# Performance work log

Measured on AMD Instinct MI355X. Metric: run time of the kernel, lower is better.

The kernel has to match this reference:

```python
import jax, jax.numpy as jnp
import numpy as np

N_NODES = 100000
N_EDGES = 600000
IN_C, HID_C, OUT_C = 128, 128, 64


def setup_inputs() -> dict:
    key = jax.random.key(0)
    k1, k2, k3, k4 = jax.random.split(key, 4)
    x = jax.random.normal(k1, (N_NODES, IN_C), dtype=jnp.float32)
    edge_index = jax.random.randint(k2, (2, N_EDGES), 0, N_NODES, dtype=jnp.int64)
    # Glorot-ish init for linear weights
    W1 = jax.random.normal(k3, (IN_C, HID_C), dtype=jnp.float32) / np.sqrt(IN_C)
    b1 = jnp.zeros((HID_C,), dtype=jnp.float32)
    W2 = jax.random.normal(k4, (HID_C, OUT_C), dtype=jnp.float32) / np.sqrt(HID_C)
    b2 = jnp.zeros((OUT_C,), dtype=jnp.float32)
    prelu_a = jnp.full((1,), 0.25, dtype=jnp.float32)  # torch nn.PReLU default
    return {"x": x, "edge_index": edge_index, "W1": W1, "b1": b1,
            "W2": W2, "b2": b2, "prelu_a": prelu_a}


def _gcn_conv(x, src, dst, norm, W, b, num_nodes):
    # PyG GCNConv: h = x W; out[i] = sum_{(j->i)} norm_ji * h[j] + b
    h = x @ W                                   # [N, C_out]
    msg = h[src] * norm[:, None]                # [E', C_out] gather + scale
    out = jax.ops.segment_sum(msg, dst, num_segments=num_nodes)
    return out + b


def reference(x, edge_index, W1, b1, W2, b2, prelu_a):
    n = x.shape[0]
    # add self-loops
    loops = jnp.arange(n, dtype=edge_index.dtype)
    src = jnp.concatenate([edge_index[0], loops])
    dst = jnp.concatenate([edge_index[1], loops])
    # symmetric normalization deg^{-1/2}[src] * deg^{-1/2}[dst]
    deg = jax.ops.segment_sum(jnp.ones_like(dst, dtype=x.dtype), dst, num_segments=n)
    dinv = jnp.where(deg > 0, jax.lax.rsqrt(deg), 0.0)
    norm = dinv[src] * dinv[dst]
    # dropout p=0.0 -> identity
    h = _gcn_conv(x, src, dst, norm, W1, b1, n)
    h = jnp.where(h >= 0, h, prelu_a * h)       # PReLU (single shared parameter)
    out = _gcn_conv(h, src, dst, norm, W2, b2, n)
    return out
```

## Files before the change

kernel.cpp:

```cpp
#include <hip/hip_runtime.h>


typedef __attribute__((ext_vector_type(8))) short bf16x8;
typedef __attribute__((ext_vector_type(4))) float f32x4;

#define CAP 32

__device__ inline unsigned short f2bf(float f) {
    unsigned int b = __float_as_uint(f);
    b += 0x7FFFu + ((b >> 16) & 1u);
    return (unsigned short)(b >> 16);
}
__device__ inline float bflo(unsigned int u) { return __uint_as_float(u << 16); }
__device__ inline float bfhi(unsigned int u) { return __uint_as_float(u & 0xFFFF0000u); }

__global__ void k_pre(const float* __restrict__ W1, const float* __restrict__ W2,
                      unsigned short* __restrict__ Wt1, unsigned short* __restrict__ Wt2,
                      int* __restrict__ cnt, int n) {
    int i = blockIdx.x * blockDim.x + threadIdx.x;
    if (i < n) cnt[i] = 0;
    if (i < 128 * 128) {
        int nn = i >> 7, k = i & 127;
        Wt1[i] = f2bf(W1[k * 128 + nn]);
    } else if (i < 128 * 128 + 64 * 128) {
        int j = i - 128 * 128;
        int nn = j >> 7, k = j & 127;
        Wt2[j] = f2bf(W2[k * 64 + nn]);
    }
}

template <int BN, bool CVT, bool FILL>
__global__ __launch_bounds__(512) void k_gemm_mfma(
    const void* __restrict__ Asrc, const unsigned short* __restrict__ Wt,
    unsigned short* __restrict__ H, int n,
    const int* __restrict__ esrc, const int* __restrict__ edst,
    int* __restrict__ cnt, int* __restrict__ bucket, int e) {
    constexpr int PITCH = 136;
    __shared__ unsigned short Bs[BN * PITCH];
    const int tid = threadIdx.x;

    for (int q = tid; q < BN * 16; q += 512) {
        int row = q >> 4, c16 = q & 15;
        *(uint4*)(Bs + row * PITCH + c16 * 8) =
            *(const uint4*)(Wt + row * 128 + c16 * 8);
    }

    const int wave = tid >> 6, lane = tid & 63;
    const int ml = lane & 15;
    const int g = lane >> 4;
    const int stripe = blockIdx.x * 8 + wave;

    int ra = stripe * 16 + ml;
    if (ra >= n) ra = n - 1;

    bf16x8 af[4];
    if (CVT) {
        const float* A = (const float*)Asrc;
#pragma unroll
        for (int ks = 0; ks < 4; ++ks) {
            const float* p = A + (size_t)ra * 128 + ks * 32 + g * 8;
            float4 a0 = *(const float4*)p;
            float4 a1 = *(const float4*)(p + 4);
            uint4 pk;
            pk.x = (unsigned)f2bf(a0.x) | ((unsigned)f2bf(a0.y) << 16);
            pk.y = (unsigned)f2bf(a0.z) | ((unsigned)f2bf(a0.w) << 16);
            pk.z = (unsigned)f2bf(a1.x) | ((unsigned)f2bf(a1.y) << 16);
            pk.w = (unsigned)f2bf(a1.z) | ((unsigned)f2bf(a1.w) << 16);
            af[ks] = *(bf16x8*)&pk;
        }
    } else {
        const unsigned short* A = (const unsigned short*)Asrc;
#pragma unroll
        for (int ks = 0; ks < 4; ++ks)
            af[ks] = *(const bf16x8*)(A + (size_t)ra * 128 + ks * 32 + g * 8);
    }

    if (FILL) {
        for (int i = blockIdx.x * 512 + tid; i < e; i += gridDim.x * 512) {
            int d = edst[i];
            int s = esrc[i];
            int pos = atomicAdd(&cnt[d], 1);
            if (pos < CAP) bucket[(size_t)d * CAP + pos] = s;
        }
    }

    __syncthreads();

    constexpr int NCT = BN / 16;
    f32x4 acc[NCT];
#pragma unroll
    for (int ct = 0; ct < NCT; ++ct) acc[ct] = (f32x4){0.f, 0.f, 0.f, 0.f};

#pragma unroll
    for (int ks = 0; ks < 4; ++ks)
#pragma unroll
        for (int ct = 0; ct < NCT; ++ct) {
            bf16x8 b = *(const bf16x8*)(Bs + (size_t)(ct * 16 + ml) * PITCH + ks * 32 + g * 8);
            acc[ct] = __builtin_amdgcn_mfma_f32_16x16x32_bf16(af[ks], b, acc[ct], 0, 0, 0);
        }

#pragma unroll
    for (int ct = 0; ct < NCT; ++ct)
#pragma unroll
        for (int reg = 0; reg < 4; ++reg) {
            int r = stripe * 16 + g * 4 + reg;
            if (r < n) H[(size_t)r * BN + ct * 16 + ml] = f2bf(acc[ct][reg]);
        }
}

template <int COLS, bool PRELU_BF16_OUT>
__global__ void k_gather(const unsigned short* __restrict__ H,
                         const int* __restrict__ cnt, const int* __restrict__ bucket,
                         const float* __restrict__ b, void* __restrict__ outp,
                         const float* __restrict__ alpha_p, int n) {
    constexpr int NT = COLS / 8;
    constexpr int G = 256 / NT;
    const int tid = threadIdx.x;
    const int node = blockIdx.x * G + tid / NT;
    if (node >= n) return;
    const int c0 = (tid & (NT - 1)) * 8;

    int c = cnt[node];
    const float di = rsqrtf(1.0f + (float)c);
    if (c > CAP) c = CAP;

    float acc[8];
    {
        uint4 v = *(const uint4*)(H + (size_t)node * COLS + c0);
        float sl = di * di;
        acc[0] = bflo(v.x) * sl + b[c0 + 0];
        acc[1] = bfhi(v.x) * sl + b[c0 + 1];
        acc[2] = bflo(v.y) * sl + b[c0 + 2];
        acc[3] = bfhi(v.y) * sl + b[c0 + 3];
        acc[4] = bflo(v.z) * sl + b[c0 + 4];
        acc[5] = bfhi(v.z) * sl + b[c0 + 5];
        acc[6] = bflo(v.w) * sl + b[c0 + 6];
        acc[7] = bfhi(v.w) * sl + b[c0 + 7];
    }

    const int* bp = bucket + (size_t)node * CAP;
    const int nb4 = (c + 3) >> 2;
    for (int q = 0; q < nb4; ++q) {
        int4 idx = *(const int4*)(bp + q * 4);
        int base = q * 4;
        int s0 = idx.x;
        int s1 = (base + 1 < c) ? idx.y : s0;
        int s2 = (base + 2 < c) ? idx.z : s0;
        int s3 = (base + 3 < c) ? idx.w : s0;
        int cn0 = cnt[s0], cn1 = cnt[s1], cn2 = cnt[s2], cn3 = cnt[s3];
        uint4 v0 = *(const uint4*)(H + (size_t)s0 * COLS + c0);
        uint4 v1 = *(const uint4*)(H + (size_t)s1 * COLS + c0);
        uint4 v2 = *(const uint4*)(H + (size_t)s2 * COLS + c0);
        uint4 v3 = *(const uint4*)(H + (size_t)s3 * COLS + c0);
        float n0 = rsqrtf(1.0f + (float)cn0) * di;
        float n1 = (base + 1 < c) ? rsqrtf(1.0f + (float)cn1) * di : 0.0f;
        float n2 = (base + 2 < c) ? rsqrtf(1.0f + (float)cn2) * di : 0.0f;
        float n3 = (base + 3 < c) ? rsqrtf(1.0f + (float)cn3) * di : 0.0f;
        acc[0] += bflo(v0.x) * n0; acc[1] += bfhi(v0.x) * n0;
        acc[2] += bflo(v0.y) * n0; acc[3] += bfhi(v0.y) * n0;
        acc[4] += bflo(v0.z) * n0; acc[5] += bfhi(v0.z) * n0;
        acc[6] += bflo(v0.w) * n0; acc[7] += bfhi(v0.w) * n0;
        acc[0] += bflo(v1.x) * n1; acc[1] += bfhi(v1.x) * n1;
        acc[2] += bflo(v1.y) * n1; acc[3] += bfhi(v1.y) * n1;
        acc[4] += bflo(v1.z) * n1; acc[5] += bfhi(v1.z) * n1;
        acc[6] += bflo(v1.w) * n1; acc[7] += bfhi(v1.w) * n1;
        acc[0] += bflo(v2.x) * n2; acc[1] += bfhi(v2.x) * n2;
        acc[2] += bflo(v2.y) * n2; acc[3] += bfhi(v2.y) * n2;
        acc[4] += bflo(v2.z) * n2; acc[5] += bfhi(v2.z) * n2;
        acc[6] += bflo(v2.w) * n2; acc[7] += bfhi(v2.w) * n2;
        acc[0] += bflo(v3.x) * n3; acc[1] += bfhi(v3.x) * n3;
        acc[2] += bflo(v3.y) * n3; acc[3] += bfhi(v3.y) * n3;
        acc[4] += bflo(v3.z) * n3; acc[5] += bfhi(v3.z) * n3;
        acc[6] += bflo(v3.w) * n3; acc[7] += bfhi(v3.w) * n3;
    }

    if (PRELU_BF16_OUT) {
        float al = alpha_p[0];
        unsigned short o[8];
#pragma unroll
        for (int j = 0; j < 8; ++j) {
            float t = acc[j];
            t = (t >= 0.f) ? t : al * t;
            o[j] = f2bf(t);
        }
        uint4 pk;
        pk.x = (unsigned)o[0] | ((unsigned)o[1] << 16);
        pk.y = (unsigned)o[2] | ((unsigned)o[3] << 16);
        pk.z = (unsigned)o[4] | ((unsigned)o[5] << 16);
        pk.w = (unsigned)o[6] | ((unsigned)o[7] << 16);
        *(uint4*)((unsigned short*)outp + (size_t)node * COLS + c0) = pk;
    } else {
        float* out = (float*)outp;
        *(float4*)(out + (size_t)node * COLS + c0) =
            make_float4(acc[0], acc[1], acc[2], acc[3]);
        *(float4*)(out + (size_t)node * COLS + c0 + 4) =
            make_float4(acc[4], acc[5], acc[6], acc[7]);
    }
}

extern "C" void kernel_launch(void* const* d_in, const int* in_sizes, int n_in,
                              void* d_out, int out_size, void* d_ws, size_t ws_size,
                              hipStream_t stream) {
    const float* x  = (const float*)d_in[0];
    const int*   ei = (const int*)d_in[1];
    const float* W1 = (const float*)d_in[2];
    const float* b1 = (const float*)d_in[3];
    const float* W2 = (const float*)d_in[4];
    const float* b2 = (const float*)d_in[5];
    const float* pa = (const float*)d_in[6];
    float* out = (float*)d_out;

    const int n = in_sizes[0] / 128;
    const int e = in_sizes[1] / 2;
    const int* src = ei;
    const int* dst = ei + e;
    const int B = 256;

    unsigned short* h1  = (unsigned short*)d_ws;
    unsigned short* hp  = h1 + (size_t)n * 128;
    unsigned short* h2  = hp + (size_t)n * 128;
    unsigned short* Wt1 = h2 + (size_t)n * 64;
    unsigned short* Wt2 = Wt1 + 128 * 128;
    int* cnt     = (int*)(Wt2 + 64 * 128);
    int* bucket  = cnt + n;

    const int gblk = ((n + 15) / 16 + 7) / 8;

    k_pre<<<(n + B - 1) / B, B, 0, stream>>>(W1, W2, Wt1, Wt2, cnt, n);
    k_gemm_mfma<128, true, true><<<gblk, 512, 0, stream>>>(
        x, Wt1, h1, n, src, dst, cnt, bucket, e);
    k_gather<128, true><<<(n + 15) / 16, 256, 0, stream>>>(h1, cnt, bucket,
                                                           b1, hp, pa, n);
    k_gemm_mfma<64, false, false><<<gblk, 512, 0, stream>>>(
        hp, Wt2, h2, n, nullptr, nullptr, nullptr, nullptr, 0);
    k_gather<64, false><<<(n + 31) / 32, 256, 0, stream>>>(h2, cnt, bucket,
                                                           b2, out, nullptr, n);
}
```

Measured before the change: 195.3 us.

## Fuse layer-1 gather and PReLU into layer-2 GEMM; split edge fill into dedicated blocks

Moves the layer-1 neighbor aggregation, bias, and PReLU into the second MFMA GEMM kernel, so each lane gathers its A-fragment directly from H1 and the hp intermediate is never written or re-read. The edge bucket fill now runs in a dedicated set of 320 blocks inside the first GEMM launch, instead of being interleaved with the GEMM work in every block. This removes one kernel launch and a round trip of an N×128 bf16 buffer. In exchange, the fused gather runs with the GEMM's 16-row-per-wave lane layout, which gives less memory parallelism and lower occupancy than the standalone gather kernel.

Result: no change. 198.4 us (+1.6%).

```diff
diff --git a/kernel.cpp b/kernel.cpp
--- a/kernel.cpp
+++ b/kernel.cpp
@@ -5,6 +5,7 @@
 typedef __attribute__((ext_vector_type(4))) float f32x4;
 
 #define CAP 32
+#define FILLB 320
 
 __device__ inline unsigned short f2bf(float f) {
     unsigned int b = __float_as_uint(f);
@@ -29,16 +30,26 @@
     }
 }
 
-template <int BN, bool CVT, bool FILL>
-__global__ __launch_bounds__(512) void k_gemm_mfma(
-    const void* __restrict__ Asrc, const unsigned short* __restrict__ Wt,
+__global__ __launch_bounds__(512) void k_gemm_fill(
+    const float* __restrict__ A, const unsigned short* __restrict__ Wt,
     unsigned short* __restrict__ H, int n,
     const int* __restrict__ esrc, const int* __restrict__ edst,
     int* __restrict__ cnt, int* __restrict__ bucket, int e) {
-    constexpr int PITCH = 136;
+    constexpr int BN = 128, PITCH = 136;
     __shared__ unsigned short Bs[BN * PITCH];
     const int tid = threadIdx.x;
 
+    if (blockIdx.x < FILLB) {
+        for (int i = blockIdx.x * 512 + tid; i < e; i += FILLB * 512) {
+            int d = edst[i];
+            int s = esrc[i];
+            int pos = atomicAdd(&cnt[d], 1);
+            if (pos < CAP) bucket[(size_t)d * CAP + pos] = s;
+        }
+        return;
+    }
+
+    const int bid = blockIdx.x - FILLB;
     for (int q = tid; q < BN * 16; q += 512) {
         int row = q >> 4, c16 = q & 15;
         *(uint4*)(Bs + row * PITCH + c16 * 8) =
@@ -46,61 +57,39 @@
     }
 
     const int wave = tid >> 6, lane = tid & 63;
-    const int ml = lane & 15;
-    const int g = lane >> 4;
-    const int stripe = blockIdx.x * 8 + wave;
-
+    const int ml = lane & 15, g = lane >> 4;
+    const int stripe = bid * 8 + wave;
     int ra = stripe * 16 + ml;
     if (ra >= n) ra = n - 1;
 
     bf16x8 af[4];
-    if (CVT) {
-        const float* A = (const float*)Asrc;
-#pragma unroll
-        for (int ks = 0; ks < 4; ++ks) {
-            const float* p = A + (size_t)ra * 128 + ks * 32 + g * 8;
-            float4 a0 = *(const float4*)p;
-            float4 a1 = *(const float4*)(p + 4);
-            uint4 pk;
-            pk.x = (unsigned)f2bf(a0.x) | ((unsigned)f2bf(a0.y) << 16);
-            pk.y = (unsigned)f2bf(a0.z) | ((unsigned)f2bf(a0.w) << 16);
-            pk.z = (unsigned)f2bf(a1.x) | ((unsigned)f2bf(a1.y) << 16);
-            pk.w = (unsigned)f2bf(a1.z) | ((unsigned)f2bf(a1.w) << 16);
-            af[ks] = *(bf16x8*)&pk;
-        }
-    } else {
-        const unsigned short* A = (const unsigned short*)Asrc;
-#pragma unroll
-        for (int ks = 0; ks < 4; ++ks)
-            af[ks] = *(const bf16x8*)(A + (size_t)ra * 128 + ks * 32 + g * 8);
-    }
-
-    if (FILL) {
-        for (int i = blockIdx.x * 512 + tid; i < e; i += gridDim.x * 512) {
-            int d = edst[i];
-            int s = esrc[i];
-            int pos = atomicAdd(&cnt[d], 1);
-            if (pos < CAP) bucket[(size_t)d * CAP + pos] = s;
-        }
+#pragma unroll
+    for (int ks = 0; ks < 4; ++ks) {
+        const float* p = A + (size_t)ra * 128 + ks * 32 + g * 8;
+        float4 a0 = *(const float4*)p;
+        float4 a1 = *(const float4*)(p + 4);
+        uint4 pk;
+        pk.x = (unsigned)f2bf(a0.x) | ((unsigned)f2bf(a0.y) << 16);
+        pk.y = (unsigned)f2bf(a0.z) | ((unsigned)f2bf(a0.w) << 16);
+        pk.z = (unsigned)f2bf(a1.x) | ((unsigned)f2bf(a1.y) << 16);
+        pk.w = (unsigned)f2bf(a1.z) | ((unsigned)f2bf(a1.w) << 16);
+        af[ks] = *(bf16x8*)&pk;
     }
 
     __syncthreads();
 
-    constexpr int NCT = BN / 16;
-    f32x4 acc[NCT];
-#pragma unroll
-    for (int ct = 0; ct < NCT; ++ct) acc[ct] = (f32x4){0.f, 0.f, 0.f, 0.f};
-
+    f32x4 acc[8];
+#pragma unroll
+    for (int ct = 0; ct < 8; ++ct) acc[ct] = (f32x4){0.f, 0.f, 0.f, 0.f};
 #pragma unroll
     for (int ks = 0; ks < 4; ++ks)
 #pragma unroll
-        for (int ct = 0; ct < NCT; ++ct) {
+        for (int ct = 0; ct < 8; ++ct) {
             bf16x8 b = *(const bf16x8*)(Bs + (size_t)(ct * 16 + ml) * PITCH + ks * 32 + g * 8);
             acc[ct] = __builtin_amdgcn_mfma_f32_16x16x32_bf16(af[ks], b, acc[ct], 0, 0, 0);
         }
-
-#pragma unroll
-    for (int ct = 0; ct < NCT; ++ct)
+#pragma unroll
+    for (int ct = 0; ct < 8; ++ct)
 #pragma unroll
         for (int reg = 0; reg < 4; ++reg) {
             int r = stripe * 16 + g * 4 + reg;
@@ -108,13 +97,137 @@
         }
 }
 
-template <int COLS, bool PRELU_BF16_OUT>
-__global__ void k_gather(const unsigned short* __restrict__ H,
-                         const int* __restrict__ cnt, const int* __restrict__ bucket,
-                         const float* __restrict__ b, void* __restrict__ outp,
-                         const float* __restrict__ alpha_p, int n) {
-    constexpr int NT = COLS / 8;
-    constexpr int G = 256 / NT;
+__global__ __launch_bounds__(512) void k_gemm2_fused(
+    const unsigned short* __restrict__ H1, const unsigned short* __restrict__ Wt2,
+    const int* __restrict__ cnt, const int* __restrict__ bucket,
+    const float* __restrict__ b1, const float* __restrict__ alpha_p,
+    unsigned short* __restrict__ H2, int n) {
+    constexpr int BN = 64, PITCH = 136;
+    __shared__ unsigned short Bs[BN * PITCH];
+    const int tid = threadIdx.x;
+
+    for (int q = tid; q < BN * 16; q += 512) {
+        int row = q >> 4, c16 = q & 15;
+        *(uint4*)(Bs + row * PITCH + c16 * 8) =
+            *(const uint4*)(Wt2 + row * 128 + c16 * 8);
+    }
+
+    const int wave = tid >> 6, lane = tid & 63;
+    const int ml = lane & 15, g = lane >> 4;
+    const int stripe = blockIdx.x * 8 + wave;
+    int ra = stripe * 16 + ml;
+    if (ra >= n) ra = n - 1;
+
+    int c = cnt[ra];
+    const float di = rsqrtf(1.0f + (float)c);
+    if (c > CAP) c = CAP;
+    const float sl = di * di;
+
+    float acc[4][8];
+#pragma unroll
+    for (int ks = 0; ks < 4; ++ks) {
+        uint4 v = *(const uint4*)(H1 + (size_t)ra * 128 + ks * 32 + g * 8);
+        const float* bb = b1 + ks * 32 + g * 8;
+        acc[ks][0] = bflo(v.x) * sl + bb[0];
+        acc[ks][1] = bfhi(v.x) * sl + bb[1];
+        acc[ks][2] = bflo(v.y) * sl + bb[2];
+        acc[ks][3] = bfhi(v.y) * sl + bb[3];
+        acc[ks][4] = bflo(v.z) * sl + bb[4];
+        acc[ks][5] = bfhi(v.z) * sl + bb[5];
+        acc[ks][6] = bflo(v.w) * sl + bb[6];
+        acc[ks][7] = bfhi(v.w) * sl + bb[7];
+    }
+
+    const int* bp = bucket + (size_t)ra * CAP;
+    int q = 0;
+    for (; q + 2 <= c; q += 2) {
+        int s0 = bp[q], s1 = bp[q + 1];
+        int cn0 = cnt[s0], cn1 = cnt[s1];
+        uint4 u0[4], u1[4];
+#pragma unroll
+        for (int ks = 0; ks < 4; ++ks) {
+            u0[ks] = *(const uint4*)(H1 + (size_t)s0 * 128 + ks * 32 + g * 8);
+            u1[ks] = *(const uint4*)(H1 + (size_t)s1 * 128 + ks * 32 + g * 8);
+        }
+        float n0 = rsqrtf(1.0f + (float)cn0) * di;
+        float n1 = rsqrtf(1.0f + (float)cn1) * di;
+#pragma unroll
+        for (int ks = 0; ks < 4; ++ks) {
+            acc[ks][0] += bflo(u0[ks].x) * n0 + bflo(u1[ks].x) * n1;
+            acc[ks][1] += bfhi(u0[ks].x) * n0 + bfhi(u1[ks].x) * n1;
+            acc[ks][2] += bflo(u0[ks].y) * n0 + bflo(u1[ks].y) * n1;
+            acc[ks][3] += bfhi(u0[ks].y) * n0 + bfhi(u1[ks].y) * n1;
+            acc[ks][4] += bflo(u0[ks].z) * n0 + bflo(u1[ks].z) * n1;
+            acc[ks][5] += bfhi(u0[ks].z) * n0 + bfhi(u1[ks].z) * n1;
+            acc[ks][6] += bflo(u0[ks].w) * n0 + bflo(u1[ks].w) * n1;
+            acc[ks][7] += bfhi(u0[ks].w) * n0 + bfhi(u1[ks].w) * n1;
+        }
+    }
+    if (q < c) {
+        int s0 = bp[q];
+        int cn0 = cnt[s0];
+        uint4 u0[4];
+#pragma unroll
+        for (int ks = 0; ks < 4; ++ks)
+            u0[ks] = *(const uint4*)(H1 + (size_t)s0 * 128 + ks * 32 + g * 8);
+        float n0 = rsqrtf(1.0f + (float)cn0) * di;
+#pragma unroll
+        for (int ks = 0; ks < 4; ++ks) {
+            acc[ks][0] += bflo(u0[ks].x) * n0;
+            acc[ks][1] += bfhi(u0[ks].x) * n0;
+            acc[ks][2] += bflo(u0[ks].y) * n0;
+            acc[ks][3] += bfhi(u0[ks].y) * n0;
+            acc[ks][4] += bflo(u0[ks].z) * n0;
+            acc[ks][5] += bfhi(u0[ks].z) * n0;
+            acc[ks][6] += bflo(u0[ks].w) * n0;
+            acc[ks][7] += bfhi(u0[ks].w) * n0;
+        }
+    }
+
+    const float al = alpha_p[0];
+    bf16x8 af[4];
+#pragma unroll
+    for (int ks = 0; ks < 4; ++ks) {
+        unsigned short o[8];
+#pragma unroll
+        for (int j = 0; j < 8; ++j) {
+            float t = acc[ks][j];
+            t = (t >= 0.f) ? t : al * t;
+            o[j] = f2bf(t);
+        }
+        uint4 pk;
+        pk.x = (unsigned)o[0] | ((unsigned)o[1] << 16);
+        pk.y = (unsigned)o[2] | ((unsigned)o[3] << 16);
+        pk.z = (unsigned)o[4] | ((unsigned)o[5] << 16);
+        pk.w = (unsigned)o[6] | ((unsigned)o[7] << 16);
+        af[ks] = *(bf16x8*)&pk;
+    }
+
+    __syncthreads();
+
+    f32x4 dacc[4];
+#pragma unroll
+    for (int ct = 0; ct < 4; ++ct) dacc[ct] = (f32x4){0.f, 0.f, 0.f, 0.f};
+#pragma unroll
+    for (int ks = 0; ks < 4; ++ks)
+#pragma unroll
+        for (int ct = 0; ct < 4; ++ct) {
+            bf16x8 b = *(const bf16x8*)(Bs + (size_t)(ct * 16 + ml) * PITCH + ks * 32 + g * 8);
+            dacc[ct] = __builtin_amdgcn_mfma_f32_16x16x32_bf16(af[ks], b, dacc[ct], 0, 0, 0);
+        }
+#pragma unroll
+    for (int ct = 0; ct < 4; ++ct)
+#pragma unroll
+        for (int reg = 0; reg < 4; ++reg) {
+            int r = stripe * 16 + g * 4 + reg;
+            if (r < n) H2[(size_t)r * BN + ct * 16 + ml] = f2bf(dacc[ct][reg]);
+        }
+}
+
+__global__ void k_gather2(const unsigned short* __restrict__ H,
+                          const int* __restrict__ cnt, const int* __restrict__ bucket,
+                          const float* __restrict__ b, float* __restrict__ out, int n) {
+    constexpr int COLS = 64, NT = COLS / 8, G = 256 / NT;
     const int tid = threadIdx.x;
     const int node = blockIdx.x * G + tid / NT;
     if (node >= n) return;
@@ -174,28 +287,10 @@
         acc[6] += bflo(v3.w) * n3; acc[7] += bfhi(v3.w) * n3;
     }
 
-    if (PRELU_BF16_OUT) {
-        float al = alpha_p[0];
-        unsigned short o[8];
-#pragma unroll
-        for (int j = 0; j < 8; ++j) {
-            float t = acc[j];
-            t = (t >= 0.f) ? t : al * t;
-            o[j] = f2bf(t);
-        }
-        uint4 pk;
-        pk.x = (unsigned)o[0] | ((unsigned)o[1] << 16);
-        pk.y = (unsigned)o[2] | ((unsigned)o[3] << 16);
-        pk.z = (unsigned)o[4] | ((unsigned)o[5] << 16);
-        pk.w = (unsigned)o[6] | ((unsigned)o[7] << 16);
-        *(uint4*)((unsigned short*)outp + (size_t)node * COLS + c0) = pk;
-    } else {
-        float* out = (float*)outp;
-        *(float4*)(out + (size_t)node * COLS + c0) =
-            make_float4(acc[0], acc[1], acc[2], acc[3]);
-        *(float4*)(out + (size_t)node * COLS + c0 + 4) =
-            make_float4(acc[4], acc[5], acc[6], acc[7]);
-    }
+    *(float4*)(out + (size_t)node * COLS + c0) =
+        make_float4(acc[0], acc[1], acc[2], acc[3]);
+    *(float4*)(out + (size_t)node * COLS + c0 + 4) =
+        make_float4(acc[4], acc[5], acc[6], acc[7]);
 }
 
 extern "C" void kernel_launch(void* const* d_in, const int* in_sizes, int n_in,
@@ -217,8 +312,7 @@
     const int B = 256;
 
     unsigned short* h1  = (unsigned short*)d_ws;
-    unsigned short* hp  = h1 + (size_t)n * 128;
-    unsigned short* h2  = hp + (size_t)n * 128;
+    unsigned short* h2  = h1 + (size_t)n * 128;
     unsigned short* Wt1 = h2 + (size_t)n * 64;
     unsigned short* Wt2 = Wt1 + 128 * 128;
     int* cnt     = (int*)(Wt2 + 64 * 128);
@@ -227,12 +321,8 @@
     const int gblk = ((n + 15) / 16 + 7) / 8;
 
     k_pre<<<(n + B - 1) / B, B, 0, stream>>>(W1, W2, Wt1, Wt2, cnt, n);
-    k_gemm_mfma<128, true, true><<<gblk, 512, 0, stream>>>(
-        x, Wt1, h1, n, src, dst, cnt, bucket, e);
-    k_gather<128, true><<<(n + 15) / 16, 256, 0, stream>>>(h1, cnt, bucket,
-                                                           b1, hp, pa, n);
-    k_gemm_mfma<64, false, false><<<gblk, 512, 0, stream>>>(
-        hp, Wt2, h2, n, nullptr, nullptr, nullptr, nullptr, 0);
-    k_gather<64, false><<<(n + 31) / 32, 256, 0, stream>>>(h2, cnt, bucket,
-                                                           b2, out, nullptr, n);
-}
+    k_gemm_fill<<<gblk + FILLB, 512, 0, stream>>>(x, Wt1, h1, n,
+                                                  src, dst, cnt, bucket, e);
+    k_gemm2_fused<<<gblk, 512, 0, stream>>>(h1, Wt2, cnt, bucket, b1, pa, h2, n);
+    k_gather2<<<(n + 31) / 32, 256, 0, stream>>>(h2, cnt, bucket, b2, out, n);
+}
```
